# Optimization experiments

Measured on AMD Instinct MI355X. Metric: run time of the kernel, lower is better.

## Reference

```python
import jax, jax.numpy as jnp
import numpy as np

EPS = 1e-8


def setup_inputs() -> dict:
    key = jax.random.key(0)
    k1, k2, k3, k4 = jax.random.split(key, 4)
    B, C, H, W = 16, 256, 32, 32
    E, V = 512, 8192
    x = jax.random.normal(k1, (B, C, H, W), dtype=jnp.float32)
    w_pre = jax.random.normal(k2, (E, C), dtype=jnp.float32) * 0.05
    b_pre = jax.random.normal(k3, (E,), dtype=jnp.float32) * 0.05
    # embedding init mirrors uniform_(-1/vocab, 1/vocab)
    embedding = jax.random.uniform(k4, (V, E), dtype=jnp.float32, minval=-1.0 / V, maxval=1.0 / V)
    return {"x": x, "w_pre": w_pre, "b_pre": b_pre, "embedding": embedding}


def reference(x, w_pre, b_pre, embedding):
    B, C, H, W = x.shape
    V, E = embedding.shape
    # pre_quant_conv: 1x1 Conv2d == per-pixel linear over channels
    z = jnp.einsum('bchw,ec->behw', x, w_pre) + b_pre[None, :, None, None]  # [B,E,H,W]
    # flatten to (b h w, e)
    z_flat = z.transpose(0, 2, 3, 1).reshape(-1, E)  # [BHW, E]
    zn = z_flat / (EPS + jnp.linalg.norm(z_flat, axis=1, keepdims=True))
    en = embedding / (EPS + jnp.linalg.norm(embedding, axis=1, keepdims=True))
    sims = zn @ en.T  # [BHW, V]
    tokens = jnp.argmax(sims, axis=-1)  # [BHW]
    z_q = embedding[tokens].reshape(B, H, W, E).transpose(0, 3, 1, 2)  # [B,E,H,W]
    # straight-through norm-blend from Tokenizer.forward
    normed_z = z / (EPS + jnp.linalg.norm(z, axis=1, keepdims=True))
    norm_zq = EPS + jnp.linalg.norm(z_q, axis=1, keepdims=True)
    normed_zq = z_q / norm_zq
    decoder_input = (normed_z + jax.lax.stop_gradient(normed_zq - normed_z)) * norm_zq
    return z, z_q, decoder_input, tokens.reshape(B, H * W)
```

## Files before the change

kernel.cpp:

```cpp
#include <hip/hip_runtime.h>
#include <math.h>

#define EPSF 1e-8f
#define MARGIN 4e-3f

constexpr int Bn = 16, Cc = 256, HW = 1024, Ee = 512, Vv = 8192;
constexpr int Mm = Bn * HW;

constexpr long O_Z   = 0;
constexpr long O_ZQ  = 8388608;
constexpr long O_DEC = 16777216;
constexpr long O_TOK = 25165824;

typedef __attribute__((ext_vector_type(8))) short s16x8;
typedef __attribute__((ext_vector_type(4))) short s16x4;
typedef __attribute__((ext_vector_type(8))) _Float16 f16x8;
typedef __attribute__((ext_vector_type(4))) float f32x4;

__device__ __forceinline__ unsigned short f2h(float x) {
    _Float16 h = (_Float16)x;
    return __builtin_bit_cast(unsigned short, h);
}
__device__ __forceinline__ float h2f(unsigned short b) {
    return (float)__builtin_bit_cast(_Float16, b);
}


__global__ void k_prep(const float* __restrict__ w, float* __restrict__ wT,
                       const float* __restrict__ emb, float* __restrict__ en_inv,
                       float* __restrict__ en_norm, unsigned short* __restrict__ Bhi,
                       int* __restrict__ cnt) {
    int b = blockIdx.x, t = threadIdx.x;
    int v = b * 4 + (t >> 6);
    int lane = t & 63;
    const float* row = emb + (long)v * Ee + lane * 8;
    float4 d0 = *(const float4*)row;
    float4 d1 = *(const float4*)(row + 4);
    float s = 0.f;
    s = fmaf(d0.x, d0.x, s); s = fmaf(d0.y, d0.y, s);
    s = fmaf(d0.z, d0.z, s); s = fmaf(d0.w, d0.w, s);
    s = fmaf(d1.x, d1.x, s); s = fmaf(d1.y, d1.y, s);
    s = fmaf(d1.z, d1.z, s); s = fmaf(d1.w, d1.w, s);
#pragma unroll
    for (int off = 32; off; off >>= 1) s += __shfl_xor(s, off);
    float n = sqrtf(s);
    float inv = 1.0f / (EPSF + n);
    if (lane == 0) { en_norm[v] = EPSF + n; en_inv[v] = inv; }
    s16x8 h;
    h[0] = (short)f2h(d0.x * inv); h[1] = (short)f2h(d0.y * inv);
    h[2] = (short)f2h(d0.z * inv); h[3] = (short)f2h(d0.w * inv);
    h[4] = (short)f2h(d1.x * inv); h[5] = (short)f2h(d1.y * inv);
    h[6] = (short)f2h(d1.z * inv); h[7] = (short)f2h(d1.w * inv);
    *(s16x8*)(Bhi + (long)v * Ee + lane * 8) = h;
    if (b < 512) {
        int gid = b * 256 + t;
        int c = gid >> 9, e = gid & 511;
        wT[gid] = w[e * Cc + c];
    } else if (b < 576) {
        cnt[(b - 512) * 256 + t] = 0;
    }
}


__global__ __launch_bounds__(256) void k_gemm1(const float* __restrict__ x,
                                               const float* __restrict__ wT,
                                               const float* __restrict__ bias,
                                               float* __restrict__ z,
                                               unsigned short* __restrict__ Ahi,
                                               unsigned short* __restrict__ Alo,
                                               float* __restrict__ sumsq_part) {
    __shared__ float As[32][128];
    __shared__ float Bs[32][128];
    int m0 = blockIdx.x * 128;
    int b = m0 >> 10, hw0 = m0 & 1023;
    int e0 = blockIdx.y * 128;
    int t = threadIdx.x;
    int mi = t >> 4, ni = t & 15;
    float acc[8][8] = {};
    for (int c0 = 0; c0 < Cc; c0 += 32) {
#pragma unroll
        for (int q = 0; q < 4; ++q) {
            int f = t + 256 * q;
            int kk = f >> 5, p4 = (f & 31) * 4;
            *(float4*)&As[kk][p4] = *(const float4*)(x + ((long)(b * Cc + c0 + kk)) * HW + hw0 + p4);
            *(float4*)&Bs[kk][p4] = *(const float4*)(wT + (long)(c0 + kk) * Ee + e0 + p4);
        }
        __syncthreads();
#pragma unroll
        for (int kk = 0; kk < 32; ++kk) {
            float av[8], bv[8];
            *(float4*)&av[0] = *(float4*)&As[kk][mi * 8];
            *(float4*)&av[4] = *(float4*)&As[kk][mi * 8 + 4];
            *(float4*)&bv[0] = *(float4*)&Bs[kk][ni * 8];
            *(float4*)&bv[4] = *(float4*)&Bs[kk][ni * 8 + 4];
#pragma unroll
            for (int r = 0; r < 8; ++r)
#pragma unroll
                for (int c = 0; c < 8; ++c) acc[r][c] = fmaf(av[r], bv[c], acc[r][c]);
        }
        __syncthreads();
    }
    float ov[8][8];
#pragma unroll
    for (int c = 0; c < 8; ++c) {
        int e = e0 + ni * 8 + c;
        float be = bias[e];
#pragma unroll
        for (int r = 0; r < 8; ++r) ov[r][c] = acc[r][c] + be;
        float4 o0 = make_float4(ov[0][c], ov[1][c], ov[2][c], ov[3][c]);
        float4 o1 = make_float4(ov[4][c], ov[5][c], ov[6][c], ov[7][c]);
        float* zp = z + ((long)(b * Ee + e)) * HW + hw0 + mi * 8;
        *(float4*)zp = o0;
        *(float4*)(zp + 4) = o1;
    }
    float sq[8];
#pragma unroll
    for (int r = 0; r < 8; ++r) {
        s16x8 h, lo;
        float s = 0.f;
#pragma unroll
        for (int c = 0; c < 8; ++c) {
            unsigned short hh = f2h(ov[r][c]);
            h[c]  = (short)hh;
            lo[c] = (short)f2h(ov[r][c] - h2f(hh));
            s = fmaf(ov[r][c], ov[r][c], s);
        }
        sq[r] = s;
        long off = (long)(m0 + mi * 8 + r) * Ee + e0 + ni * 8;
        *(s16x8*)(Ahi + off) = h;
        *(s16x8*)(Alo + off) = lo;
    }
#pragma unroll
    for (int r = 0; r < 8; ++r)
#pragma unroll
        for (int off = 1; off < 16; off <<= 1) sq[r] += __shfl_xor(sq[r], off);
    if (ni == 0) {
#pragma unroll
        for (int r = 0; r < 8; ++r)
            sumsq_part[(long)(m0 + mi * 8 + r) * 4 + blockIdx.y] = sq[r];
    }
}


__global__ void k_norm(const float* __restrict__ sumsq_part, float* __restrict__ norm,
                       float* __restrict__ inv_zn) {
    int p = blockIdx.x * 256 + threadIdx.x;
    const float* sp = sumsq_part + (long)p * 4;
    float s = (sp[0] + sp[1]) + (sp[2] + sp[3]);
    float nv = EPSF + sqrtf(s);
    norm[p] = nv;
    inv_zn[p] = 1.0f / nv;
}


__global__ __launch_bounds__(256, 4) void k_sims(const unsigned short* __restrict__ Ahi,
                                                 const unsigned short* __restrict__ Bhi,
                                                 const float* __restrict__ norm,
                                                 float* __restrict__ part_v,
                                                 int* __restrict__ part_i,
                                                 float2* __restrict__ extras,
                                                 int* __restrict__ cnt) {
    __shared__ short As[8192];
    __shared__ short Bs[8192];
    __shared__ float red_v[2][2][64];
    __shared__ int   red_i[2][2][64];
    __shared__ float red_m[2][64];
    __shared__ int   red_wi[2][64];

    int t = threadIdx.x;
    int wg = blockIdx.x;
    int xcd = wg & 7, r = wg >> 3;
    int bx = xcd * 16 + (r & 15);
    int by = r >> 4;
    long m0 = (long)bx * 128, n0 = (long)by * 128;

    int wid = t >> 6, l = t & 63;
    int wr = wid >> 1, wc = wid & 1;
    int l15 = l & 15, lg = l >> 4;

    auto stage = [&](const unsigned short* gbase, short* region, long row0, int k0) {
#pragma unroll
        for (int j = 0; j < 4; ++j) {
            int i = j * 256 + t;
            int rr = i >> 3, s = i & 7;
            int sp = s ^ (rr & 7);
            const unsigned short* gp = gbase + (row0 + rr) * Ee + k0 + sp * 8;
            short* lp = region + (long)(j * 256 + (t & ~63)) * 8;
            __builtin_amdgcn_global_load_lds(
                (const __attribute__((address_space(1))) unsigned int*)gp,
                (__attribute__((address_space(3))) unsigned int*)lp, 16, 0, 0);
        }
    };

    f32x4 acc[4][4];
#pragma unroll
    for (int i = 0; i < 4; ++i)
#pragma unroll
        for (int j = 0; j < 4; ++j) acc[i][j] = (f32x4){0.f, 0.f, 0.f, 0.f};

    stage(Ahi, As, m0, 0);
    stage(Bhi, Bs, n0, 0);

    for (int kt = 0; kt < 8; ++kt) {
        __syncthreads();
        s16x8 af[4][2], bf[4][2];
#pragma unroll
        for (int mt = 0; mt < 4; ++mt)
#pragma unroll
            for (int kk = 0; kk < 2; ++kk) {
                int row = wr * 64 + mt * 16 + l15;
                int g = kk * 4 + lg;
                af[mt][kk] = *(const s16x8*)&As[row * 64 + ((g ^ (row & 7)) * 8)];
                int nrow = wc * 64 + mt * 16 + l15;
                bf[mt][kk] = *(const s16x8*)&Bs[nrow * 64 + ((g ^ (nrow & 7)) * 8)];
            }
        __syncthreads();
        if (kt < 7) {
            stage(Ahi, As, m0, (kt + 1) * 64);
            stage(Bhi, Bs, n0, (kt + 1) * 64);
        }
#pragma unroll
        for (int kk = 0; kk < 2; ++kk)
#pragma unroll
            for (int mt = 0; mt < 4; ++mt)
#pragma unroll
                for (int nt = 0; nt < 4; ++nt)
                    acc[mt][nt] = __builtin_amdgcn_mfma_f32_16x16x32_f16(
                        __builtin_bit_cast(f16x8, af[mt][kk]),
                        __builtin_bit_cast(f16x8, bf[nt][kk]), acc[mt][nt], 0, 0, 0);
    }

#pragma unroll
    for (int mt = 0; mt < 4; ++mt)
#pragma unroll
        for (int rg = 0; rg < 4; ++rg) {
            float best = -3e38f; int bi = 0x7FFFFFFF;
#pragma unroll
            for (int nt = 0; nt < 4; ++nt) {
                float val = acc[mt][nt][rg];
                int idx = (int)n0 + wc * 64 + nt * 16 + l15;
                if (val > best) { best = val; bi = idx; }
            }
#pragma unroll
            for (int off = 1; off < 16; off <<= 1) {
                float ov = __shfl_xor(best, off);
                int oi = __shfl_xor(bi, off);
                if (ov > best || (ov == best && oi < bi)) { best = ov; bi = oi; }
            }
            if (l15 == 0) {
                int rloc = mt * 16 + lg * 4 + rg;
                red_v[wr][wc][rloc] = best;
                red_i[wr][wc][rloc] = bi;
            }
        }
    __syncthreads();
    if (t < 128) {
        int wr_ = t >> 6, rloc = t & 63;
        float va = red_v[wr_][0][rloc]; int ia = red_i[wr_][0][rloc];
        float vb = red_v[wr_][1][rloc]; int ib = red_i[wr_][1][rloc];
        if (vb > va || (vb == va && ib < ia)) { va = vb; ia = ib; }
        long m = m0 + wr_ * 64 + rloc;
        part_v[m * 64 + by] = va;
        part_i[m * 64 + by] = ia;
        red_m[wr_][rloc] = va;
        red_wi[wr_][rloc] = ia;
    }
    __syncthreads();
#pragma unroll
    for (int mt = 0; mt < 4; ++mt)
#pragma unroll
        for (int rg = 0; rg < 4; ++rg) {
            int rloc = mt * 16 + lg * 4 + rg;
            float bm = red_m[wr][rloc];
            int wi_ = red_wi[wr][rloc];
            long p = m0 + wr * 64 + rloc;
            float thr = bm - MARGIN * norm[p];
#pragma unroll
            for (int nt = 0; nt < 4; ++nt) {
                float val = acc[mt][nt][rg];
                int idx = (int)n0 + wc * 64 + nt * 16 + l15;
                if (val >= thr && idx != wi_) {
                    int slot = atomicAdd(&cnt[p], 1);
                    if (slot < 64) extras[p * 64 + slot] = make_float2(val, __int_as_float(idx));
                }
            }
        }
}


__global__ __launch_bounds__(256) void k_pick(const float* __restrict__ part_v,
                                              const int* __restrict__ part_i,
                                              const float2* __restrict__ extras,
                                              const int* __restrict__ cnt,
                                              const unsigned short* __restrict__ Ahi,
                                              const unsigned short* __restrict__ Alo,
                                              const float* __restrict__ emb,
                                              const float* __restrict__ en_inv,
                                              const float* __restrict__ norm,
                                              int* __restrict__ tok_i,
                                              float* __restrict__ tok_f) {
    int p = blockIdx.x * 4 + (threadIdx.x >> 6);
    int lane = threadIdx.x & 63;
    float wv = part_v[(long)p * 64 + lane];
    int wi = part_i[(long)p * 64 + lane];
    float m1 = wv;
#pragma unroll
    for (int off = 1; off < 64; off <<= 1) {
        float ov = __shfl_xor(m1, off);
        if (ov > m1) m1 = ov;
    }
    float thr = m1 - MARGIN * norm[p];
    int n = cnt[p]; if (n > 64) n = 64;
    float ev = -3e38f; int ei = 0;
    if (lane < n) {
        float2 e2 = extras[(long)p * 64 + lane];
        ev = e2.x; ei = __float_as_int(e2.y);
    }
    unsigned long long mw = __ballot(wv >= thr);
    unsigned long long me = __ballot(ev >= thr);
    s16x8 ah = *(const s16x8*)(Ahi + (long)p * Ee + lane * 8);
    s16x8 al = *(const s16x8*)(Alo + (long)p * Ee + lane * 8);
    float a[8];
#pragma unroll
    for (int j = 0; j < 8; ++j)
        a[j] = h2f((unsigned short)ah[j]) + h2f((unsigned short)al[j]);

    float best = -3e38f; int bi = 0x7FFFFFFF;
    auto rescore = [&](int v) {
        const float* er = emb + (long)v * Ee + lane * 8;
        float4 b0 = *(const float4*)er;
        float4 b1 = *(const float4*)(er + 4);
        float s = 0.f;
        s = fmaf(a[0], b0.x, s); s = fmaf(a[1], b0.y, s);
        s = fmaf(a[2], b0.z, s); s = fmaf(a[3], b0.w, s);
        s = fmaf(a[4], b1.x, s); s = fmaf(a[5], b1.y, s);
        s = fmaf(a[6], b1.z, s); s = fmaf(a[7], b1.w, s);
#pragma unroll
        for (int off = 1; off < 64; off <<= 1) s += __shfl_xor(s, off);
        s *= en_inv[v];
        if (s > best || (s == best && v < bi)) { best = s; bi = v; }
    };
    while (mw) {
        int b = __ffsll(mw) - 1; mw &= mw - 1;
        rescore(__shfl(wi, b));
    }
    while (me) {
        int b = __ffsll(me) - 1; me &= me - 1;
        rescore(__shfl(ei, b));
    }
    if (lane == 0) { tok_i[p] = bi; tok_f[p] = (float)bi; }
}


__global__ void k_final(const float* __restrict__ z, const float* __restrict__ emb,
                        const int* __restrict__ tok, const float* __restrict__ inv_zn,
                        const float* __restrict__ en_inv, const float* __restrict__ en_norm,
                        float* __restrict__ zq, float* __restrict__ dec) {
    long gid = (long)blockIdx.x * 256 + threadIdx.x;
    int hw = (int)(gid & 1023);
    int b  = (int)(gid >> 19);
    int p  = (b << 10) | hw;
    int e  = (int)((gid >> 10) & 511);
    int tk = tok[p];
    float zqv = emb[(long)tk * Ee + e];
    float nq  = en_norm[tk];
    float nzq = zqv * en_inv[tk];
    float zv  = z[gid];
    float nz  = zv * inv_zn[p];
    zq[gid]  = zqv;
    dec[gid] = (nz + (nzq - nz)) * nq;
}


extern "C" void kernel_launch(void* const* d_in, const int* in_sizes, int n_in,
                              void* d_out, int out_size, void* d_ws, size_t ws_size,
                              hipStream_t stream) {
    const float* x     = (const float*)d_in[0];
    const float* w_pre = (const float*)d_in[1];
    const float* b_pre = (const float*)d_in[2];
    const float* emb   = (const float*)d_in[3];

    float* out  = (float*)d_out;
    float* z    = out + O_Z;
    float* zq   = out + O_ZQ;
    float* dec  = out + O_DEC;
    float* tokf = out + O_TOK;

    unsigned short* Ahi = (unsigned short*)zq;
    unsigned short* Alo = Ahi + (long)Mm * Ee;
    unsigned short* Bhi = (unsigned short*)dec;
    float*  part_v = dec + 2 * 1024 * 1024;
    int*    part_i = (int*)(dec + 3 * 1024 * 1024);
    float2* extras = (float2*)(dec + 4 * 1024 * 1024);
    int*    cnt    = (int*)(dec + 6 * 1024 * 1024);
    float*  sumsq_part = dec + 6 * 1024 * 1024 + 32768;

    float* ws      = (float*)d_ws;
    float* wT      = ws;
    float* en_inv  = wT + 131072;
    float* en_norm = en_inv + 8192;
    float* inv_zn  = en_norm + 8192;
    int*   tok_i   = (int*)(inv_zn + 16384);
    float* norm    = (float*)(tok_i + 16384);

    k_prep<<<2048, 256, 0, stream>>>(w_pre, wT, emb, en_inv, en_norm, Bhi, cnt);
    dim3 g1(Mm / 128, Ee / 128);
    k_gemm1<<<g1, 256, 0, stream>>>(x, wT, b_pre, z, Ahi, Alo, sumsq_part);
    k_norm<<<Mm / 256, 256, 0, stream>>>(sumsq_part, norm, inv_zn);
    k_sims<<<8192, 256, 0, stream>>>(Ahi, Bhi, norm, part_v, part_i, extras, cnt);
    k_pick<<<Mm / 4, 256, 0, stream>>>(part_v, part_i, extras, cnt, Ahi, Alo, emb,
                                       en_inv, norm, tok_i, tokf);
    k_final<<<(int)(8388608 / 256), 256, 0, stream>>>(z, emb, tok_i, inv_zn, en_inv, en_norm, zq, dec);
}
```

Baseline: 442.6 us.

## Move A hi/lo split into separate transpose kernel with prenormalized rows; vectorize final

Removes the fp16 hi/lo split from the first GEMM epilogue. A new kernel rereads z through a shared-memory transpose, normalizes each row by its inverse norm, and writes the hi/lo halves, folding in the old norm kernel. Because A is now unit-normalized, the margin threshold no longer scales by the row norm in sims and pick. The final kernel processes four pixels per thread with float4 loads and stores. The cost is an extra read of z in exchange for a lighter GEMM epilogue and fewer kernels.

```diff
diff --git a/kernel.cpp b/kernel.cpp
--- a/kernel.cpp
+++ b/kernel.cpp
@@ -66,8 +66,6 @@
                                                const float* __restrict__ wT,
                                                const float* __restrict__ bias,
                                                float* __restrict__ z,
-                                               unsigned short* __restrict__ Ahi,
-                                               unsigned short* __restrict__ Alo,
                                                float* __restrict__ sumsq_part) {
     __shared__ float As[32][128];
     __shared__ float Bs[32][128];
@@ -116,19 +114,10 @@
     float sq[8];
 #pragma unroll
     for (int r = 0; r < 8; ++r) {
-        s16x8 h, lo;
         float s = 0.f;
 #pragma unroll
-        for (int c = 0; c < 8; ++c) {
-            unsigned short hh = f2h(ov[r][c]);
-            h[c]  = (short)hh;
-            lo[c] = (short)f2h(ov[r][c] - h2f(hh));
-            s = fmaf(ov[r][c], ov[r][c], s);
-        }
+        for (int c = 0; c < 8; ++c) s = fmaf(ov[r][c], ov[r][c], s);
         sq[r] = s;
-        long off = (long)(m0 + mi * 8 + r) * Ee + e0 + ni * 8;
-        *(s16x8*)(Ahi + off) = h;
-        *(s16x8*)(Alo + off) = lo;
     }
 #pragma unroll
     for (int r = 0; r < 8; ++r)
@@ -142,20 +131,53 @@
 }
 
 
-__global__ void k_norm(const float* __restrict__ sumsq_part, float* __restrict__ norm,
-                       float* __restrict__ inv_zn) {
-    int p = blockIdx.x * 256 + threadIdx.x;
-    const float* sp = sumsq_part + (long)p * 4;
-    float s = (sp[0] + sp[1]) + (sp[2] + sp[3]);
-    float nv = EPSF + sqrtf(s);
-    norm[p] = nv;
-    inv_zn[p] = 1.0f / nv;
+__global__ void k_Asplit(const float* __restrict__ z, const float* __restrict__ sumsq_part,
+                         unsigned short* __restrict__ Ahi, unsigned short* __restrict__ Alo,
+                         float* __restrict__ inv_zn) {
+    __shared__ float tile[64][65];
+    __shared__ float inv_s[64];
+    int p0 = (blockIdx.x >> 3) * 64;
+    int e0 = (blockIdx.x & 7) * 64;
+    int b = p0 >> 10, hw0 = p0 & 1023;
+    int t = threadIdx.x;
+    if (t < 64) {
+        const float* sp = sumsq_part + (long)(p0 + t) * 4;
+        float s = (sp[0] + sp[1]) + (sp[2] + sp[3]);
+        float inv = 1.0f / (EPSF + sqrtf(s));
+        inv_s[t] = inv;
+        if ((blockIdx.x & 7) == 0) inv_zn[p0 + t] = inv;
+    }
+#pragma unroll
+    for (int q = 0; q < 4; ++q) {
+        int f = t + 256 * q;
+        int e_l = f >> 4, p4 = (f & 15) * 4;
+        float4 d = *(const float4*)(z + ((long)(b * Ee + e0 + e_l)) * HW + hw0 + p4);
+        tile[e_l][p4 + 0] = d.x; tile[e_l][p4 + 1] = d.y;
+        tile[e_l][p4 + 2] = d.z; tile[e_l][p4 + 3] = d.w;
+    }
+    __syncthreads();
+#pragma unroll
+    for (int q = 0; q < 4; ++q) {
+        int f = t + 256 * q;
+        int p_l = f >> 4, e4 = (f & 15) * 4;
+        float inv = inv_s[p_l];
+        s16x4 h, lo;
+#pragma unroll
+        for (int j = 0; j < 4; ++j) {
+            float xv = tile[e4 + j][p_l] * inv;
+            unsigned short hh = f2h(xv);
+            h[j]  = (short)hh;
+            lo[j] = (short)f2h(xv - h2f(hh));
+        }
+        long off = (long)(p0 + p_l) * Ee + e0 + e4;
+        *(s16x4*)(Ahi + off) = h;
+        *(s16x4*)(Alo + off) = lo;
+    }
 }
 
 
 __global__ __launch_bounds__(256, 4) void k_sims(const unsigned short* __restrict__ Ahi,
                                                  const unsigned short* __restrict__ Bhi,
-                                                 const float* __restrict__ norm,
                                                  float* __restrict__ part_v,
                                                  int* __restrict__ part_i,
                                                  float2* __restrict__ extras,
@@ -274,7 +296,7 @@
             float bm = red_m[wr][rloc];
             int wi_ = red_wi[wr][rloc];
             long p = m0 + wr * 64 + rloc;
-            float thr = bm - MARGIN * norm[p];
+            float thr = bm - MARGIN;
 #pragma unroll
             for (int nt = 0; nt < 4; ++nt) {
                 float val = acc[mt][nt][rg];
@@ -296,7 +318,6 @@
                                               const unsigned short* __restrict__ Alo,
                                               const float* __restrict__ emb,
                                               const float* __restrict__ en_inv,
-                                              const float* __restrict__ norm,
                                               int* __restrict__ tok_i,
                                               float* __restrict__ tok_f) {
     int p = blockIdx.x * 4 + (threadIdx.x >> 6);
@@ -309,7 +330,7 @@
         float ov = __shfl_xor(m1, off);
         if (ov > m1) m1 = ov;
     }
-    float thr = m1 - MARGIN * norm[p];
+    float thr = m1 - MARGIN;
     int n = cnt[p]; if (n > 64) n = 64;
     float ev = -3e38f; int ei = 0;
     if (lane < n) {
@@ -356,19 +377,28 @@
                         const int* __restrict__ tok, const float* __restrict__ inv_zn,
                         const float* __restrict__ en_inv, const float* __restrict__ en_norm,
                         float* __restrict__ zq, float* __restrict__ dec) {
-    long gid = (long)blockIdx.x * 256 + threadIdx.x;
-    int hw = (int)(gid & 1023);
-    int b  = (int)(gid >> 19);
-    int p  = (b << 10) | hw;
-    int e  = (int)((gid >> 10) & 511);
-    int tk = tok[p];
-    float zqv = emb[(long)tk * Ee + e];
-    float nq  = en_norm[tk];
-    float nzq = zqv * en_inv[tk];
-    float zv  = z[gid];
-    float nz  = zv * inv_zn[p];
-    zq[gid]  = zqv;
-    dec[gid] = (nz + (nzq - nz)) * nq;
+    long u = (long)blockIdx.x * 256 + threadIdx.x;
+    int hw4 = (int)(u & 255) * 4;
+    int e   = (int)((u >> 8) & 511);
+    int b   = (int)(u >> 17);
+    long gid = ((long)(b * Ee + e)) * HW + hw4;
+    int pb = (b << 10) | hw4;
+    float4 zv = *(const float4*)(z + gid);
+    float zvv[4] = {zv.x, zv.y, zv.z, zv.w};
+    float zqv[4], dcv[4];
+#pragma unroll
+    for (int j = 0; j < 4; ++j) {
+        int p = pb + j;
+        int tk = tok[p];
+        float q  = emb[(long)tk * Ee + e];
+        float nq  = en_norm[tk];
+        float nzq = q * en_inv[tk];
+        float nz  = zvv[j] * inv_zn[p];
+        zqv[j] = q;
+        dcv[j] = (nz + (nzq - nz)) * nq;
+    }
+    *(float4*)(zq + gid)  = make_float4(zqv[0], zqv[1], zqv[2], zqv[3]);
+    *(float4*)(dec + gid) = make_float4(dcv[0], dcv[1], dcv[2], dcv[3]);
 }
 
 
@@ -401,14 +431,13 @@
     float* en_norm = en_inv + 8192;
     float* inv_zn  = en_norm + 8192;
     int*   tok_i   = (int*)(inv_zn + 16384);
-    float* norm    = (float*)(tok_i + 16384);
 
     k_prep<<<2048, 256, 0, stream>>>(w_pre, wT, emb, en_inv, en_norm, Bhi, cnt);
     dim3 g1(Mm / 128, Ee / 128);
-    k_gemm1<<<g1, 256, 0, stream>>>(x, wT, b_pre, z, Ahi, Alo, sumsq_part);
-    k_norm<<<Mm / 256, 256, 0, stream>>>(sumsq_part, norm, inv_zn);
-    k_sims<<<8192, 256, 0, stream>>>(Ahi, Bhi, norm, part_v, part_i, extras, cnt);
+    k_gemm1<<<g1, 256, 0, stream>>>(x, wT, b_pre, z, sumsq_part);
+    k_Asplit<<<2048, 256, 0, stream>>>(z, sumsq_part, Ahi, Alo, inv_zn);
+    k_sims<<<8192, 256, 0, stream>>>(Ahi, Bhi, part_v, part_i, extras, cnt);
     k_pick<<<Mm / 4, 256, 0, stream>>>(part_v, part_i, extras, cnt, Ahi, Alo, emb,
-                                       en_inv, norm, tok_i, tokf);
-    k_final<<<(int)(8388608 / 256), 256, 0, stream>>>(z, emb, tok_i, inv_zn, en_inv, en_norm, zq, dec);
-}
+                                       en_inv, tok_i, tokf);
+    k_final<<<8192, 256, 0, stream>>>(z, emb, tok_i, inv_zn, en_inv, en_norm, zq, dec);
+}
```

Result: faster. 420.7 us (-4.9%).
